# Optimization experiments

Hardware: AMD Instinct MI355X
Metric: run time of the kernel (lower is better)

The kernel has to match this reference:

```python
import jax, jax.numpy as jnp
import numpy as np

EPS = 1e-5
NEG_SLOPE = 0.2  # GATConv default negative_slope


def layer_norm(x, g, b):
    mu = jnp.mean(x, axis=-1, keepdims=True)
    var = jnp.mean((x - mu) ** 2, axis=-1, keepdims=True)
    return (x - mu) * jax.lax.rsqrt(var + EPS) * g + b


def setup_inputs() -> dict:
    key = jax.random.key(0)
    ks = jax.random.split(key, 16)
    B, NPG = 64, 1024          # graphs, fine nodes per graph
    NF = B * NPG               # 65536 fine nodes
    IN, HID, ATT, H, LLM = 1024, 1024, 64, 8, 2048
    D = ATT * H                # 512
    w = lambda k, shp: (jax.random.normal(k, shp, jnp.float32) * 0.02)
    # structured bipartite star edges: fine node i -> global node i // NPG
    edge_index = jnp.stack([jnp.arange(NF, dtype=jnp.int32),
                            (jnp.arange(NF, dtype=jnp.int32) // NPG)])
    return {
        "x_fine": jax.random.normal(ks[0], (NF, IN), jnp.float32),
        "x_global": jax.random.normal(ks[1], (B, D), jnp.float32),
        "edge_index_fine_global": edge_index,
        "nf_g": jnp.ones((IN,), jnp.float32), "nf_b": jnp.zeros((IN,), jnp.float32),
        "ip_w1": w(ks[2], (IN, HID)), "ip_b1": jnp.zeros((HID,), jnp.float32),
        "ip_w2": w(ks[3], (HID, D)), "ip_b2": jnp.zeros((D,), jnp.float32),
        "ng_g": jnp.ones((D,), jnp.float32), "ng_b": jnp.zeros((D,), jnp.float32),
        "gat_ws": w(ks[4], (D, D)), "gat_wd": w(ks[5], (D, D)),
        "att_s": w(ks[6], (1, H, ATT)), "att_d": w(ks[7], (1, H, ATT)),
        "gat_bias": jnp.zeros((D,), jnp.float32),
        "gp_w": w(ks[8], (D, LLM)), "gp_b": jnp.zeros((LLM,), jnp.float32),
        "fp_w": w(ks[9], (D, LLM)), "fp_b": jnp.zeros((LLM,), jnp.float32),
    }


def reference(x_fine, x_global, edge_index_fine_global,
              nf_g, nf_b, ip_w1, ip_b1, ip_w2, ip_b2, ng_g, ng_b,
              gat_ws, gat_wd, att_s, att_d, gat_bias,
              gp_w, gp_b, fp_w, fp_b):
    B = x_global.shape[0]
    H = att_s.shape[1]
    C = x_global.shape[1] // H

    # fine branch: LayerNorm -> MLP projection to H*C
    xf = layer_norm(x_fine, nf_g, nf_b)
    xf = jax.nn.relu(xf @ ip_w1 + ip_b1) @ ip_w2 + ip_b2      # [NF, H*C]
    xg = layer_norm(x_global, ng_g, ng_b)                      # [B, H*C]

    # bipartite GATConv (eval mode: attention dropout disabled)
    xs = (xf @ gat_ws).reshape(-1, H, C)                       # [NF, H, C]
    xd = (xg @ gat_wd).reshape(B, H, C)                        # [B, H, C]
    a_s = jnp.sum(xs * att_s, axis=-1)                         # [NF, H]
    a_d = jnp.sum(xd * att_d, axis=-1)                         # [B, H]

    row, col = edge_index_fine_global[0], edge_index_fine_global[1]
    loops = jnp.arange(B, dtype=row.dtype)                     # add_self_loops: nodes < min(NF,B)
    rows = jnp.concatenate([row, loops])
    cols = jnp.concatenate([col, loops])
    # PyG removes pre-existing self-loop edges; emulate by masking them out
    self_mask = jnp.concatenate([row == col, jnp.zeros((B,), bool)])

    logits = jax.nn.leaky_relu(a_s[rows] + a_d[cols], NEG_SLOPE)   # [E+B, H]
    logits = jnp.where(self_mask[:, None], -jnp.inf, logits)
    m = jax.ops.segment_max(logits, cols, num_segments=B)         # [B, H]
    e = jnp.exp(logits - m[cols])
    e = jnp.where(self_mask[:, None], 0.0, e)
    denom = jax.ops.segment_sum(e, cols, num_segments=B)
    alpha = e / denom[cols]                                       # [E+B, H]

    msg = xs[rows] * alpha[..., None]                              # [E+B, H, C]
    agg = jax.ops.segment_sum(msg, cols, num_segments=B)          # [B, H, C]
    xg = agg.reshape(B, H * C) + gat_bias + xg                    # GAT out + residual

    og = (xg @ gp_w + gp_b)[:, None, :]                            # [B, 1, LLM]
    of = (xf @ fp_w + fp_b).reshape(B, -1, fp_w.shape[1])          # [B, NPG, LLM]
    return jnp.concatenate([og, of], axis=1)                       # [B, 1+NPG, LLM]
```

## Files before the change

### kernel.cpp

```cpp
#include <hip/hip_runtime.h>
#include <hip/hip_bf16.h>
#include <math.h>

typedef __bf16 bf16_t;
typedef bf16_t bf16x8 __attribute__((ext_vector_type(8)));
typedef bf16_t bf16x4 __attribute__((ext_vector_type(4)));
typedef float f32x4 __attribute__((ext_vector_type(4)));

#define DEVINL __device__ __forceinline__

DEVINL float wave_reduce_sum(float v) {
#pragma unroll
  for (int o = 32; o > 0; o >>= 1) v += __shfl_down(v, o);
  return v;
}
DEVINL float wave_reduce_max(float v) {
#pragma unroll
  for (int o = 32; o > 0; o >>= 1) v = fmaxf(v, __shfl_down(v, o));
  return v;
}
DEVINL float block_reduce_sum256(float v, float* red) {
  int tid = threadIdx.x;
  __syncthreads();
  v = wave_reduce_sum(v);
  if ((tid & 63) == 0) red[tid >> 6] = v;
  __syncthreads();
  return red[0] + red[1] + red[2] + red[3];
}
DEVINL float block_reduce_max256(float v, float* red) {
  int tid = threadIdx.x;
  __syncthreads();
  v = wave_reduce_max(v);
  if ((tid & 63) == 0) red[tid >> 6] = v;
  __syncthreads();
  return fmaxf(fmaxf(red[0], red[1]), fmaxf(red[2], red[3]));
}

template <int CPT, bool BF16OUT>
__global__ __launch_bounds__(256) void k_ln(const float* __restrict__ x,
                                            const float* __restrict__ g,
                                            const float* __restrict__ b,
                                            void* __restrict__ out) {
  constexpr int COLS = CPT * 256;
  __shared__ float red[8];
  const size_t row = blockIdx.x;
  const float* xr = x + row * COLS;
  const int c0 = threadIdx.x * CPT;
  float v[CPT];
#pragma unroll
  for (int j = 0; j < CPT; j++) v[j] = xr[c0 + j];
  float s = 0;
#pragma unroll
  for (int j = 0; j < CPT; j++) s += v[j];
  const float mu = block_reduce_sum256(s, red) * (1.0f / COLS);
  float q = 0;
#pragma unroll
  for (int j = 0; j < CPT; j++) { float d = v[j] - mu; q += d * d; }
  const float var = block_reduce_sum256(q, red) * (1.0f / COLS);
  const float rs = rsqrtf(var + 1e-5f);
  if constexpr (BF16OUT) {
    bf16x4 o;
#pragma unroll
    for (int j = 0; j < CPT; j++)
      o[j] = (bf16_t)((v[j] - mu) * rs * g[c0 + j] + b[c0 + j]);
    *(bf16x4*)((bf16_t*)out + row * COLS + c0) = o;
  } else {
#pragma unroll
    for (int j = 0; j < CPT; j++)
      ((float*)out)[row * COLS + c0 + j] = (v[j] - mu) * rs * g[c0 + j] + b[c0 + j];
  }
}

__global__ __launch_bounds__(256) void k_tcast(const float* __restrict__ src,
                                               bf16_t* __restrict__ dst, int K, int N) {
  __shared__ float t[32][33];
  const int n0 = blockIdx.x * 32, k0 = blockIdx.y * 32;
  const int tx = threadIdx.x, ty = threadIdx.y;
#pragma unroll
  for (int i = 0; i < 32; i += 8)
    t[ty + i][tx] = src[(size_t)(k0 + ty + i) * N + n0 + tx];
  __syncthreads();
#pragma unroll
  for (int i = 0; i < 32; i += 8)
    dst[(size_t)(n0 + ty + i) * K + k0 + tx] = (bf16_t)t[tx][ty + i];
}

__global__ __launch_bounds__(256) void k_fold_wd(const float* __restrict__ gat_wd,
                                                 const float* __restrict__ att_d,
                                                 float* __restrict__ wd_att) {
  const int k = blockIdx.x * 256 + threadIdx.x;
#pragma unroll
  for (int h = 0; h < 8; h++) {
    float s = 0;
    for (int c = 0; c < 64; c++)
      s += gat_wd[(size_t)k * 512 + h * 64 + c] * att_d[h * 64 + c];
    wd_att[k * 8 + h] = s;
  }
}

template <int N, int K, int EPI>
__global__ __launch_bounds__(256, 2) void gemm_bt(const bf16_t* __restrict__ A,
                                                  const bf16_t* __restrict__ Bt,
                                                  const float* __restrict__ bias,
                                                  void* __restrict__ Cout) {
  __shared__ bf16_t As[128 * 64];
  __shared__ bf16_t Bs[128 * 64];
  const int tid = threadIdx.x;
  const int lane = tid & 63;
  const int wid = tid >> 6;
  const int wm = wid >> 1, wn = wid & 1;
  const size_t arow0 = (size_t)blockIdx.x * 128;
  const int bcol0 = blockIdx.y * 128;

  f32x4 acc[4][4] = {};
  const int kTiles = K / 64;
  for (int kt = 0; kt < kTiles; ++kt) {
    const int k0 = kt * 64;
#pragma unroll
    for (int i = 0; i < 4; ++i) {
      const int c = i * 256 + tid;
      const int r = c >> 3, kc = (c & 7) * 8;
      const bf16_t* ga = A + (arow0 + r) * K + k0 + kc;
      __builtin_amdgcn_global_load_lds(
          (const __attribute__((address_space(1))) void*)ga,
          (__attribute__((address_space(3))) void*)(As + c * 8), 16, 0, 0);
      const bf16_t* gb = Bt + ((size_t)bcol0 + r) * K + k0 + kc;
      __builtin_amdgcn_global_load_lds(
          (const __attribute__((address_space(1))) void*)gb,
          (__attribute__((address_space(3))) void*)(Bs + c * 8), 16, 0, 0);
    }
    __syncthreads();
#pragma unroll
    for (int kk = 0; kk < 2; ++kk) {
      bf16x8 af[4], bfr[4];
      const int kofs = kk * 32 + (lane >> 4) * 8;
#pragma unroll
      for (int m = 0; m < 4; ++m)
        af[m] = *(const bf16x8*)(As + (wm * 64 + m * 16 + (lane & 15)) * 64 + kofs);
#pragma unroll
      for (int n = 0; n < 4; ++n)
        bfr[n] = *(const bf16x8*)(Bs + (wn * 64 + n * 16 + (lane & 15)) * 64 + kofs);
#pragma unroll
      for (int m = 0; m < 4; ++m)
#pragma unroll
        for (int n = 0; n < 4; ++n)
          acc[m][n] = __builtin_amdgcn_mfma_f32_16x16x32_bf16(af[m], bfr[n], acc[m][n], 0, 0, 0);
    }
    __syncthreads();
  }
  const int lr = (lane >> 4) * 4;
  const int lc = lane & 15;
#pragma unroll
  for (int n = 0; n < 4; ++n) {
    const int col = bcol0 + wn * 64 + n * 16 + lc;
    const float bv = (EPI == 2) ? 0.0f : bias[col];
#pragma unroll
    for (int m = 0; m < 4; ++m) {
#pragma unroll
      for (int j = 0; j < 4; ++j) {
        const size_t row = arow0 + wm * 64 + m * 16 + lr + j;
        float v = acc[m][n][j] + bv;
        if constexpr (EPI == 0) v = v > 0.0f ? v : 0.0f;
        if constexpr (EPI == 3) {
          const size_t orow = row + (row >> 10) + 1;
          ((float*)Cout)[orow * (size_t)N + col] = v;
        } else {
          ((bf16_t*)Cout)[row * (size_t)N + col] = (bf16_t)v;
        }
      }
    }
  }
}

__global__ __launch_bounds__(256) void k_attn(const bf16_t* __restrict__ xs,
                                              const float* __restrict__ xg,
                                              const float* __restrict__ wd_att,
                                              const float* __restrict__ att_s,
                                              float* __restrict__ agg) {
  const int b = blockIdx.x >> 3, h = blockIdx.x & 7;
  const int tid = threadIdx.x;
  __shared__ float sl[1024];
  __shared__ float part[256];
  __shared__ float red[8];
  __shared__ float s_att[64];
  __shared__ float s_sc[4];
  if (tid < 64) s_att[tid] = att_s[h * 64 + tid];
  float pa = 0;
#pragma unroll
  for (int kk = 0; kk < 2; kk++) {
    const int k = tid + kk * 256;
    pa += xg[b * 512 + k] * wd_att[k * 8 + h];
  }
  const float a_d = block_reduce_sum256(pa, red);
  const bf16_t* xsb = xs + ((size_t)b * 1024) * 512 + h * 64;
#pragma unroll
  for (int j = 0; j < 4; j++) {
    const int i = tid + j * 256;
    const bf16_t* xr = xsb + (size_t)i * 512;
    float s = 0;
#pragma unroll
    for (int c = 0; c < 64; c += 8) {
      bf16x8 v = *(const bf16x8*)(xr + c);
#pragma unroll
      for (int u = 0; u < 8; u++) s += (float)v[u] * s_att[c + u];
    }
    const float lg = s + a_d;
    sl[i] = lg > 0.0f ? lg : 0.2f * lg;
  }
  if (tid == 0) {
    float self_lg = -INFINITY;
    if (b != 0) {
      const bf16_t* xr = xs + (size_t)b * 512 + h * 64;
      float s = 0;
      for (int c = 0; c < 64; c++) s += (float)xr[c] * s_att[c];
      const float lg = s + a_d;
      self_lg = lg > 0.0f ? lg : 0.2f * lg;
    }
    s_sc[0] = self_lg;
  }
  __syncthreads();
  float mx = -1e30f;
#pragma unroll
  for (int j = 0; j < 4; j++) mx = fmaxf(mx, sl[tid + j * 256]);
  mx = block_reduce_max256(mx, red);
  const float m = fmaxf(mx, s_sc[0]);
  float ps = 0;
#pragma unroll
  for (int j = 0; j < 4; j++) {
    const int i = tid + j * 256;
    const float e = __expf(sl[i] - m);
    sl[i] = e;
    ps += e;
  }
  if (tid == 0) s_sc[1] = __expf(s_sc[0] - m);
  const float dsum = block_reduce_sum256(ps, red);
  const float e_self = s_sc[1];
  const float inv = 1.0f / (dsum + e_self);
  const int c = tid & 63, grp = tid >> 6;
  float acc = 0;
  const bf16_t* xcol = xs + ((size_t)b * 1024) * 512 + h * 64 + c;
  for (int i = grp * 256; i < grp * 256 + 256; i++)
    acc += sl[i] * (float)xcol[(size_t)i * 512];
  if (grp == 0) acc += e_self * (float)xs[(size_t)b * 512 + h * 64 + c];
  part[tid] = acc;
  __syncthreads();
  if (tid < 64) {
    const float t = part[tid] + part[tid + 64] + part[tid + 128] + part[tid + 192];
    agg[(size_t)b * 512 + h * 64 + tid] = t * inv;
  }
}

__global__ __launch_bounds__(256) void k_og(const float* __restrict__ agg,
                                            const float* __restrict__ gat_bias,
                                            const float* __restrict__ xg,
                                            const float* __restrict__ gp_w,
                                            const float* __restrict__ gp_b,
                                            float* __restrict__ out) {
  __shared__ float xv[512];
  const int b = blockIdx.y;
  const int c = blockIdx.x * 256 + threadIdx.x;
  for (int k = threadIdx.x; k < 512; k += 256)
    xv[k] = agg[b * 512 + k] + gat_bias[k] + xg[b * 512 + k];
  __syncthreads();
  float acc = gp_b[c];
#pragma unroll 8
  for (int k = 0; k < 512; k++) acc += xv[k] * gp_w[(size_t)k * 2048 + c];
  out[(size_t)b * 1025 * 2048 + c] = acc;
}

extern "C" void kernel_launch(void* const* d_in, const int* in_sizes, int n_in,
                              void* d_out, int out_size, void* d_ws, size_t ws_size,
                              hipStream_t stream) {
  const float* x_fine   = (const float*)d_in[0];
  const float* x_global = (const float*)d_in[1];
  const float* nf_g  = (const float*)d_in[3];
  const float* nf_b  = (const float*)d_in[4];
  const float* ip_w1 = (const float*)d_in[5];
  const float* ip_b1 = (const float*)d_in[6];
  const float* ip_w2 = (const float*)d_in[7];
  const float* ip_b2 = (const float*)d_in[8];
  const float* ng_g  = (const float*)d_in[9];
  const float* ng_b  = (const float*)d_in[10];
  const float* gat_ws   = (const float*)d_in[11];
  const float* gat_wd   = (const float*)d_in[12];
  const float* att_s    = (const float*)d_in[13];
  const float* att_d    = (const float*)d_in[14];
  const float* gat_bias = (const float*)d_in[15];
  const float* gp_w = (const float*)d_in[16];
  const float* gp_b = (const float*)d_in[17];
  const float* fp_w = (const float*)d_in[18];
  const float* fp_b = (const float*)d_in[19];
  float* out = (float*)d_out;

  char* ws = (char*)d_ws;
  bf16_t* xf_ln = (bf16_t*)ws;
  bf16_t* hbuf  = (bf16_t*)(ws + 134217728ULL);
  char* sm = ws + 268435456ULL;
  bf16_t* w1t = (bf16_t*)sm;
  bf16_t* w2t = (bf16_t*)(sm + 2097152ULL);
  bf16_t* wst = (bf16_t*)(sm + 3145728ULL);
  bf16_t* fpt = (bf16_t*)(sm + 3670016ULL);
  float*  xg  = (float*)(sm + 5767168ULL);
  float*  wd_att = (float*)(sm + 5898240ULL);
  float*  aggp   = (float*)(sm + 5914624ULL);
  bf16_t* xf  = xf_ln;
  bf16_t* xsb = hbuf;

  k_tcast<<<dim3(32, 32), dim3(32, 8), 0, stream>>>(ip_w1, w1t, 1024, 1024);
  k_tcast<<<dim3(16, 32), dim3(32, 8), 0, stream>>>(ip_w2, w2t, 1024, 512);
  k_tcast<<<dim3(16, 16), dim3(32, 8), 0, stream>>>(gat_ws, wst, 512, 512);
  k_tcast<<<dim3(64, 16), dim3(32, 8), 0, stream>>>(fp_w, fpt, 512, 2048);
  k_fold_wd<<<2, 256, 0, stream>>>(gat_wd, att_d, wd_att);

  k_ln<4, true><<<65536, 256, 0, stream>>>(x_fine, nf_g, nf_b, xf_ln);
  k_ln<2, false><<<64, 256, 0, stream>>>(x_global, ng_g, ng_b, xg);

  gemm_bt<1024, 1024, 0><<<dim3(512, 8), 256, 0, stream>>>(xf_ln, w1t, ip_b1, hbuf);
  gemm_bt<512, 1024, 1><<<dim3(512, 4), 256, 0, stream>>>(hbuf, w2t, ip_b2, xf);
  gemm_bt<512, 512, 2><<<dim3(512, 4), 256, 0, stream>>>(xf, wst, nullptr, xsb);

  k_attn<<<512, 256, 0, stream>>>(xsb, xg, wd_att, att_s, aggp);
  k_og<<<dim3(8, 64), 256, 0, stream>>>(aggp, gat_bias, xg, gp_w, gp_b, out);

  gemm_bt<2048, 512, 3><<<dim3(512, 16), 256, 0, stream>>>(xf, fpt, fp_b, out);
}
```

Measured before the change: 849.1 us.

## Replace GEMM with 256x256 double-buffered 8-wave pipelined MFMA kernel

Replaces the 128x128 single-buffered GEMM with a 256x256 tile kernel using 512 threads and double-buffered LDS. Loads for the next k-tiles are issued in quarter-phases between MFMA groups. LDS reads use an XOR swizzle to avoid bank conflicts, and workgroup IDs are remapped so neighbouring blocks share tiles. The intent is to hide global-load latency, raise operand reuse and cut syncs per FLOP, at the cost of 128KB of LDS per block and heavy register pressure.

```diff
diff --git a/kernel.cpp b/kernel.cpp
--- a/kernel.cpp
+++ b/kernel.cpp
@@ -99,77 +99,134 @@
 }
 
 template <int N, int K, int EPI>
-__global__ __launch_bounds__(256, 2) void gemm_bt(const bf16_t* __restrict__ A,
-                                                  const bf16_t* __restrict__ Bt,
-                                                  const float* __restrict__ bias,
-                                                  void* __restrict__ Cout) {
-  __shared__ bf16_t As[128 * 64];
-  __shared__ bf16_t Bs[128 * 64];
-  const int tid = threadIdx.x;
-  const int lane = tid & 63;
-  const int wid = tid >> 6;
-  const int wm = wid >> 1, wn = wid & 1;
-  const size_t arow0 = (size_t)blockIdx.x * 128;
-  const int bcol0 = blockIdx.y * 128;
-
-  f32x4 acc[4][4] = {};
-  const int kTiles = K / 64;
-  for (int kt = 0; kt < kTiles; ++kt) {
-    const int k0 = kt * 64;
-#pragma unroll
-    for (int i = 0; i < 4; ++i) {
-      const int c = i * 256 + tid;
-      const int r = c >> 3, kc = (c & 7) * 8;
-      const bf16_t* ga = A + (arow0 + r) * K + k0 + kc;
-      __builtin_amdgcn_global_load_lds(
-          (const __attribute__((address_space(1))) void*)ga,
-          (__attribute__((address_space(3))) void*)(As + c * 8), 16, 0, 0);
-      const bf16_t* gb = Bt + ((size_t)bcol0 + r) * K + k0 + kc;
-      __builtin_amdgcn_global_load_lds(
-          (const __attribute__((address_space(1))) void*)gb,
-          (__attribute__((address_space(3))) void*)(Bs + c * 8), 16, 0, 0);
-    }
-    __syncthreads();
-#pragma unroll
-    for (int kk = 0; kk < 2; ++kk) {
-      bf16x8 af[4], bfr[4];
-      const int kofs = kk * 32 + (lane >> 4) * 8;
-#pragma unroll
-      for (int m = 0; m < 4; ++m)
-        af[m] = *(const bf16x8*)(As + (wm * 64 + m * 16 + (lane & 15)) * 64 + kofs);
-#pragma unroll
-      for (int n = 0; n < 4; ++n)
-        bfr[n] = *(const bf16x8*)(Bs + (wn * 64 + n * 16 + (lane & 15)) * 64 + kofs);
-#pragma unroll
-      for (int m = 0; m < 4; ++m)
-#pragma unroll
-        for (int n = 0; n < 4; ++n)
-          acc[m][n] = __builtin_amdgcn_mfma_f32_16x16x32_bf16(af[m], bfr[n], acc[m][n], 0, 0, 0);
-    }
-    __syncthreads();
-  }
-  const int lr = (lane >> 4) * 4;
-  const int lc = lane & 15;
-#pragma unroll
-  for (int n = 0; n < 4; ++n) {
-    const int col = bcol0 + wn * 64 + n * 16 + lc;
-    const float bv = (EPI == 2) ? 0.0f : bias[col];
-#pragma unroll
-    for (int m = 0; m < 4; ++m) {
-#pragma unroll
-      for (int j = 0; j < 4; ++j) {
-        const size_t row = arow0 + wm * 64 + m * 16 + lr + j;
-        float v = acc[m][n][j] + bv;
-        if constexpr (EPI == 0) v = v > 0.0f ? v : 0.0f;
-        if constexpr (EPI == 3) {
-          const size_t orow = row + (row >> 10) + 1;
-          ((float*)Cout)[orow * (size_t)N + col] = v;
-        } else {
-          ((bf16_t*)Cout)[row * (size_t)N + col] = (bf16_t)v;
+__global__ __launch_bounds__(512, 2) void gemm8p(const bf16_t* __restrict__ A,
+                                                 const bf16_t* __restrict__ Bt,
+                                                 const float* __restrict__ bias,
+                                                 void* __restrict__ Cout) {
+  __shared__ __align__(16) bf16_t As[2][16384];
+  __shared__ __align__(16) bf16_t Bs[2][16384];
+  constexpr int GX = 256;
+  constexpr int nt = K / 64;
+  constexpr int nwg = GX * (N / 256);
+  const int orig = blockIdx.x;
+  const int wg = (orig & 7) * (nwg >> 3) + (orig >> 3);
+  const int bx = wg & 255;
+  const int by = wg >> 8;
+  const int tid = threadIdx.x, lane = tid & 63, wid = tid >> 6;
+  const int wm = wid >> 2, wn = wid & 3;
+  const size_t arow0 = (size_t)bx * 256;
+  const int bcol0 = by * 256;
+
+  const int sr = tid >> 3;
+  const int skc = (tid & 7) ^ (sr & 7);
+  const bf16_t* gA = A + (arow0 + sr) * K + skc * 8;
+  const bf16_t* gB = Bt + ((size_t)bcol0 + sr) * K + skc * 8;
+
+  const int l15 = lane & 15, l7 = lane & 7, lq = lane >> 4;
+  const int e0 = (lq ^ l7) * 8;
+  const int e1 = ((lq ^ 4) ^ l7) * 8;
+
+  f32x4 acc[8][4] = {};
+
+#define STAGE8(ldsArr, g, h, b, kt)                                                \
+  do {                                                                             \
+    _Pragma("unroll") for (int _j = 0; _j < 2; _j++) {                             \
+      const bf16_t* _src = (g) + ((size_t)((h)*128 + _j * 64)) * K + (kt)*64;      \
+      __builtin_amdgcn_global_load_lds(                                            \
+          (const __attribute__((address_space(1))) void*)_src,                     \
+          (__attribute__((address_space(3))) void*)&ldsArr[b][(h)*8192 + tid * 8 + \
+                                                              _j * 4096],          \
+          16, 0, 0);                                                               \
+    }                                                                              \
+  } while (0)
+
+  STAGE8(As, gA, 0, 0, 0);
+  STAGE8(As, gA, 1, 0, 0);
+  STAGE8(Bs, gB, 0, 0, 0);
+  STAGE8(Bs, gB, 1, 0, 0);
+  STAGE8(Bs, gB, 0, 1, 1);
+  STAGE8(As, gA, 0, 1, 1);
+  asm volatile("s_waitcnt vmcnt(4)" ::: "memory");
+  __builtin_amdgcn_s_barrier();
+
+#define PHASE8(b, MH, NH, STAGECODE, LAST)                                       \
+  {                                                                              \
+    bf16x8 af[4][2], bfr[2][2];                                                  \
+    const bf16_t* abase = &As[b][((MH)*128 + wm * 64 + l15) * 64];               \
+    _Pragma("unroll") for (int _m = 0; _m < 4; _m++) {                           \
+      af[_m][0] = *(const bf16x8*)(abase + _m * 1024 + e0);                      \
+      af[_m][1] = *(const bf16x8*)(abase + _m * 1024 + e1);                      \
+    }                                                                            \
+    const bf16_t* bbase = &Bs[b][((NH)*128 + wn * 32 + l15) * 64];               \
+    _Pragma("unroll") for (int _n = 0; _n < 2; _n++) {                           \
+      bfr[_n][0] = *(const bf16x8*)(bbase + _n * 1024 + e0);                     \
+      bfr[_n][1] = *(const bf16x8*)(bbase + _n * 1024 + e1);                     \
+    }                                                                            \
+    STAGECODE;                                                                   \
+    __builtin_amdgcn_s_barrier();                                                \
+    __builtin_amdgcn_s_setprio(1);                                               \
+    _Pragma("unroll") for (int _m = 0; _m < 4; _m++) {                           \
+      _Pragma("unroll") for (int _n = 0; _n < 2; _n++) {                         \
+        acc[(MH)*4 + _m][(NH)*2 + _n] = __builtin_amdgcn_mfma_f32_16x16x32_bf16( \
+            af[_m][0], bfr[_n][0], acc[(MH)*4 + _m][(NH)*2 + _n], 0, 0, 0);      \
+        acc[(MH)*4 + _m][(NH)*2 + _n] = __builtin_amdgcn_mfma_f32_16x16x32_bf16( \
+            af[_m][1], bfr[_n][1], acc[(MH)*4 + _m][(NH)*2 + _n], 0, 0, 0);      \
+      }                                                                          \
+    }                                                                            \
+    __builtin_amdgcn_s_setprio(0);                                               \
+    if (LAST) asm volatile("s_waitcnt vmcnt(4)" ::: "memory");                   \
+    __builtin_amdgcn_s_barrier();                                                \
+  }
+
+  for (int t = 0; t < nt; t += 2) {
+    {
+      const int kn1 = (t + 1 < nt) ? t + 1 : nt - 1;
+      const int kn2 = (t + 2 < nt) ? t + 2 : nt - 1;
+      PHASE8(0, 0, 0, STAGE8(As, gA, 1, 1, kn1), 0)
+      PHASE8(0, 1, 0, STAGE8(Bs, gB, 1, 1, kn1), 0)
+      PHASE8(0, 0, 1, STAGE8(Bs, gB, 0, 0, kn2), 0)
+      PHASE8(0, 1, 1, STAGE8(As, gA, 0, 0, kn2), 1)
+    }
+    {
+      const int t1 = t + 1;
+      const int kn1 = (t1 + 1 < nt) ? t1 + 1 : nt - 1;
+      const int kn2 = (t1 + 2 < nt) ? t1 + 2 : nt - 1;
+      PHASE8(1, 0, 0, STAGE8(As, gA, 1, 0, kn1), 0)
+      PHASE8(1, 1, 0, STAGE8(Bs, gB, 1, 0, kn1), 0)
+      PHASE8(1, 0, 1, STAGE8(Bs, gB, 0, 1, kn2), 0)
+      PHASE8(1, 1, 1, STAGE8(As, gA, 0, 1, kn2), 1)
+    }
+  }
+
+  const int lr = lq * 4;
+#pragma unroll
+  for (int NH = 0; NH < 2; NH++) {
+#pragma unroll
+    for (int n = 0; n < 2; n++) {
+      const int col = bcol0 + NH * 128 + wn * 32 + n * 16 + l15;
+      const float bv = (EPI == 2) ? 0.0f : bias[col];
+#pragma unroll
+      for (int MH = 0; MH < 2; MH++) {
+#pragma unroll
+        for (int m = 0; m < 4; m++) {
+#pragma unroll
+          for (int j = 0; j < 4; j++) {
+            const size_t row = arow0 + MH * 128 + wm * 64 + m * 16 + lr + j;
+            float v = acc[MH * 4 + m][NH * 2 + n][j] + bv;
+            if (EPI == 0) v = v > 0.0f ? v : 0.0f;
+            if (EPI == 3) {
+              const size_t orow = row + (row >> 10) + 1;
+              ((float*)Cout)[orow * (size_t)N + col] = v;
+            } else {
+              ((bf16_t*)Cout)[row * (size_t)N + col] = (bf16_t)v;
+            }
+          }
         }
       }
     }
   }
+#undef PHASE8
+#undef STAGE8
 }
 
 __global__ __launch_bounds__(256) void k_attn(const bf16_t* __restrict__ xs,
@@ -315,12 +372,12 @@
   k_ln<4, true><<<65536, 256, 0, stream>>>(x_fine, nf_g, nf_b, xf_ln);
   k_ln<2, false><<<64, 256, 0, stream>>>(x_global, ng_g, ng_b, xg);
 
-  gemm_bt<1024, 1024, 0><<<dim3(512, 8), 256, 0, stream>>>(xf_ln, w1t, ip_b1, hbuf);
-  gemm_bt<512, 1024, 1><<<dim3(512, 4), 256, 0, stream>>>(hbuf, w2t, ip_b2, xf);
-  gemm_bt<512, 512, 2><<<dim3(512, 4), 256, 0, stream>>>(xf, wst, nullptr, xsb);
+  gemm8p<1024, 1024, 0><<<1024, 512, 0, stream>>>(xf_ln, w1t, ip_b1, hbuf);
+  gemm8p<512, 1024, 1><<<512, 512, 0, stream>>>(hbuf, w2t, ip_b2, xf);
+  gemm8p<512, 512, 2><<<512, 512, 0, stream>>>(xf, wst, nullptr, xsb);
 
   k_attn<<<512, 256, 0, stream>>>(xsb, xg, wd_att, att_s, aggp);
   k_og<<<dim3(8, 64), 256, 0, stream>>>(aggp, gat_bias, xg, gp_w, gp_b, out);
 
-  gemm_bt<2048, 512, 3><<<dim3(512, 16), 256, 0, stream>>>(xf, fpt, fp_b, out);
-}
+  gemm8p<2048, 512, 3><<<2048, 512, 0, stream>>>(xf, fpt, fp_b, out);
+}
```

Result: no change. 859.7 us (+1.3%).
